# Kernel tuning notes

Measured on AMD Instinct MI355X. Metric: run time of the kernel, lower is better.

The kernel has to match this reference:

```python
import jax, jax.numpy as jnp
import numpy as np

B, S, V, H = 256, 1024, 256, 256


def setup_inputs() -> dict:
    key = jax.random.key(0)
    ks = jax.random.split(key, 12)
    s = 1.0 / np.sqrt(H)
    def u(k, shape):
        return jax.random.uniform(k, shape, jnp.float32, -s, s)
    return {
        "x": jax.random.normal(ks[0], (B, S, V), jnp.float32),
        "w_ih0": u(ks[1], (4 * H, V)),
        "w_hh0": u(ks[2], (4 * H, H)),
        "b_ih0": u(ks[3], (4 * H,)),
        "b_hh0": u(ks[4], (4 * H,)),
        "w_ih1": u(ks[5], (4 * H, H)),
        "w_hh1": u(ks[6], (4 * H, H)),
        "b_ih1": u(ks[7], (4 * H,)),
        "b_hh1": u(ks[8], (4 * H,)),
        "fc_w": u(ks[9], (V, H)),
        "fc_b": u(ks[10], (V,)),
    }


def _lstm_layer(inp, w_ih, w_hh, b_ih, b_hh):
    # inp: [B, S, D]. Precompute input contribution for all timesteps (big GEMM),
    # then scan the recurrence (PyTorch gate order: i, f, g, o).
    pre = jnp.einsum('bsd,gd->bsg', inp, w_ih) + b_ih + b_hh  # [B, S, 4H]
    h0 = jnp.zeros((inp.shape[0], w_hh.shape[1]), inp.dtype)
    c0 = jnp.zeros_like(h0)

    def step(carry, p):
        h, c = carry
        g = p + h @ w_hh.T  # [B, 4H]
        i, f, gg, o = jnp.split(g, 4, axis=-1)
        c = jax.nn.sigmoid(f) * c + jax.nn.sigmoid(i) * jnp.tanh(gg)
        h = jax.nn.sigmoid(o) * jnp.tanh(c)
        return (h, c), h

    _, hs = jax.lax.scan(step, (h0, c0), pre.transpose(1, 0, 2))  # hs: [S, B, H]
    return hs.transpose(1, 0, 2)


def reference(x, w_ih0, w_hh0, b_ih0, b_hh0, w_ih1, w_hh1, b_ih1, b_hh1, fc_w, fc_b):
    h1 = _lstm_layer(x, w_ih0, w_hh0, b_ih0, b_hh0)
    h2 = _lstm_layer(h1, w_ih1, w_hh1, b_ih1, b_hh1)
    logits = jnp.einsum('bsh,vh->bsv', h2, fc_w) + fc_b
    return jax.nn.log_softmax(logits, axis=-1)
```

## Files before the change

kernel.cpp:

```cpp
#include <hip/hip_runtime.h>
#include <cstdint>
#include <cstddef>


typedef __attribute__((ext_vector_type(8))) short bf16x8;
typedef __attribute__((ext_vector_type(4))) float f32x4;
typedef unsigned long long ull;

#define DEVFN __device__ __forceinline__

constexpr unsigned SENT = 0xFFFFFFFFu;

DEVFN unsigned short f2bf(float f) {
  union { float f; unsigned u; } v; v.f = f;
  unsigned r = v.u + 0x7FFFu + ((v.u >> 16) & 1u);
  return (unsigned short)(r >> 16);
}
DEVFN float sigm(float x) {
  return __builtin_amdgcn_rcpf(1.f + exp2f(x * -1.442695041f));
}
DEVFN float tanh2(float x) {
  return 1.f - 2.f * __builtin_amdgcn_rcpf(1.f + exp2f(x * 2.885390082f));
}
DEVFN ull aload64(const ull* p) {
  return __hip_atomic_load(p, __ATOMIC_RELAXED, __HIP_MEMORY_SCOPE_AGENT);
}
DEVFN void astore64(ull* p, ull v) {
  __hip_atomic_store(p, v, __ATOMIC_RELAXED, __HIP_MEMORY_SCOPE_AGENT);
}
DEVFN bf16x8 fragu(ull a, ull b) {
  union { ull u[2]; bf16x8 f; } t; t.u[0] = a; t.u[1] = b; return t.f;
}
DEVFN bf16x8 frag4(uint4 u) { union { uint4 u; bf16x8 f; } t; t.u = u; return t.f; }

#define KEEP8(a0,a1,a2,a3,a4,a5,a6,a7) \
  asm volatile("" : "+v"(a0), "+v"(a1), "+v"(a2), "+v"(a3), \
                    "+v"(a4), "+v"(a5), "+v"(a6), "+v"(a7))

__global__ void pack_w(const float* __restrict__ w, unsigned short* __restrict__ dst) {
  int bid = blockIdx.x;
  int lane = threadIdx.x;
  int col = (bid >> 3) * 16 + (lane & 15);
  int k0  = (bid & 7) * 32 + (lane >> 4) * 8;
  const float* src = w + (size_t)col * 256 + k0;
  unsigned short* d = dst + ((size_t)bid * 64 + lane) * 8;
#pragma unroll
  for (int j = 0; j < 8; ++j) d[j] = f2bf(src[j]);
}

__global__ void pack_x(const float* __restrict__ x, unsigned short* __restrict__ xp) {
  int bid = blockIdx.x, lane = threadIdx.x;
  int tc = bid & 7, kt = (bid >> 3) & 7, m = bid >> 6;
  int row = lane & 15, hi = lane >> 4;
  for (int t = tc * 128; t < tc * 128 + 128; ++t) {
    const float* s = x + ((size_t)(16 * m + row) * 1024 + t) * 256 + kt * 32 + hi * 8;
    float4 f0 = *(const float4*)s;
    float4 f1 = *(const float4*)(s + 4);
    uint4 o;
    o.x = f2bf(f0.x) | ((unsigned)f2bf(f0.y) << 16);
    o.y = f2bf(f0.z) | ((unsigned)f2bf(f0.w) << 16);
    o.z = f2bf(f1.x) | ((unsigned)f2bf(f1.y) << 16);
    o.w = f2bf(f1.z) | ((unsigned)f2bf(f1.w) << 16);
    *(uint4*)(xp + ((((size_t)t * 16 + m) * 8 + kt) * 64 + lane) * 8) = o;
  }
}

__global__ __attribute__((amdgpu_flat_work_group_size(64, 64),
                          amdgpu_waves_per_eu(1, 1)))
void lstm_dual(
    const unsigned short* __restrict__ xp,
    const unsigned short* __restrict__ Wih0, const unsigned short* __restrict__ Whh0,
    const float* __restrict__ bih0, const float* __restrict__ bhh0,
    const unsigned short* __restrict__ Wih1, const unsigned short* __restrict__ Whh1,
    const float* __restrict__ bih1, const float* __restrict__ bhh1,
    unsigned short* __restrict__ h1f, unsigned short* __restrict__ h2f)
{
  __shared__ unsigned short tl[16][24];
  const int lane = threadIdx.x;
  const int bid  = (int)blockIdx.x;
  const int m = bid & 15;
  const int L = (bid >> 4) & 1;
  const int w = bid >> 5;
  const int u = w * 16 + (lane & 15);
  const bool ownlane = (((lane >> 4) >> 1) == (w & 1));
  const int  mykt = w >> 1;

  const unsigned short* Wih = L ? Wih1 : Wih0;
  const unsigned short* Whh = L ? Whh1 : Whh0;
  const float* bihp = L ? bih1 : bih0;
  const float* bhhp = L ? bhh1 : bhh0;

  bf16x8 bwih[4][8], bwhh[4][8];
#pragma unroll
  for (int g = 0; g < 4; ++g)
#pragma unroll
    for (int kt = 0; kt < 8; ++kt) {
      bwih[g][kt] = *(const bf16x8*)(Wih + ((((size_t)(g * 16 + w)) * 8 + kt) * 64 + lane) * 8);
      bwhh[g][kt] = *(const bf16x8*)(Whh + ((((size_t)(g * 16 + w)) * 8 + kt) * 64 + lane) * 8);
    }
#pragma unroll
  for (int g = 0; g < 4; ++g) {
    KEEP8(bwih[g][0], bwih[g][1], bwih[g][2], bwih[g][3],
          bwih[g][4], bwih[g][5], bwih[g][6], bwih[g][7]);
    KEEP8(bwhh[g][0], bwhh[g][1], bwhh[g][2], bwhh[g][3],
          bwhh[g][4], bwhh[g][5], bwhh[g][6], bwhh[g][7]);
  }

  float bias[4];
#pragma unroll
  for (int g = 0; g < 4; ++g) bias[g] = bihp[g * 256 + u] + bhhp[g * 256 + u];

  float c[4] = {0.f, 0.f, 0.f, 0.f};

  constexpr int TSTEP_U = 16384;
  constexpr int TSTEP_X = 8192;

  if (!L) {
    const ull* hrd  = (const ull*)h1f + m * 1024 + lane * 2;
    const ull* hrd2 = hrd + 512;
    ull* hwr = (ull*)h1f + m * 1024 + mykt * 128 + lane * 2;
    const uint4* xq  = (const uint4*)xp + m * 512 + lane;
    const uint4* xq2 = xq + 256;

    uint4 xpre[8];
#pragma unroll
    for (int kt = 0; kt < 4; ++kt) { xpre[kt] = xq[kt * 64]; xpre[4 + kt] = xq2[kt * 64]; }
    xq += TSTEP_X; xq2 += TSTEP_X;

    for (int t = 0; t < 1024; ++t) {
      ull hv[16];
      if (t > 0) {
#pragma unroll
        for (int kt = 0; kt < 4; ++kt) {
          hv[2*kt]     = aload64(hrd  + kt * 128);
          hv[2*kt + 1] = aload64(hrd  + kt * 128 + 1);
          hv[8 + 2*kt]     = aload64(hrd2 + kt * 128);
          hv[8 + 2*kt + 1] = aload64(hrd2 + kt * 128 + 1);
        }
      }

      f32x4 acc[4];
#pragma unroll
      for (int g = 0; g < 4; ++g) acc[g] = (f32x4){0.f, 0.f, 0.f, 0.f};
#pragma unroll
      for (int kt = 0; kt < 8; ++kt) {
        bf16x8 a = frag4(xpre[kt]);
#pragma unroll
        for (int g = 0; g < 4; ++g)
          acc[g] = __builtin_amdgcn_mfma_f32_16x16x32_bf16(a, bwih[g][kt], acc[g], 0, 0, 0);
      }

      if (t > 0) {
        int rounds = 0;
        while (true) {
          bool bad = false;
#pragma unroll
          for (int i = 0; i < 16; ++i) bad = bad || ((unsigned)hv[i] == SENT);
          if (!__any(bad)) break;
          if (++rounds > 8) __builtin_amdgcn_s_sleep(1);
#pragma unroll
          for (int kt = 0; kt < 4; ++kt) {
            hv[2*kt]     = aload64(hrd  + kt * 128);
            hv[2*kt + 1] = aload64(hrd  + kt * 128 + 1);
            hv[8 + 2*kt]     = aload64(hrd2 + kt * 128);
            hv[8 + 2*kt + 1] = aload64(hrd2 + kt * 128 + 1);
          }
        }
#pragma unroll
        for (int kt = 0; kt < 8; ++kt) {
          bf16x8 a = fragu(hv[kt < 4 ? 2*kt : 2*kt], hv[kt < 4 ? 2*kt+1 : 2*kt+1]);
#pragma unroll
          for (int g = 0; g < 4; ++g)
            acc[g] = __builtin_amdgcn_mfma_f32_16x16x32_bf16(a, bwhh[g][kt], acc[g], 0, 0, 0);
        }
        hrd += TSTEP_U; hrd2 += TSTEP_U;
      }

      float hq[4];
#pragma unroll
      for (int q = 0; q < 4; ++q) {
        float ia = acc[0][q] + bias[0];
        float fa = acc[1][q] + bias[1];
        float ga = acc[2][q] + bias[2];
        float oa = acc[3][q] + bias[3];
        c[q] = sigm(fa) * c[q] + sigm(ia) * tanh2(ga);
        hq[q] = sigm(oa) * tanh2(c[q]);
      }
#pragma unroll
      for (int q = 0; q < 4; ++q)
        tl[(lane >> 4) * 4 + q][lane & 15] = f2bf(hq[q]);
      uint4 nown = *(const uint4*)(&tl[lane & 15][((lane >> 4) & 1) * 8]);
      if (ownlane) {
        astore64(hwr,     ((ull)nown.y << 32) | nown.x);
        astore64(hwr + 1, ((ull)nown.w << 32) | nown.z);
      }
      hwr += TSTEP_U;

      if (t < 1023) {
#pragma unroll
        for (int kt = 0; kt < 4; ++kt) { xpre[kt] = xq[kt * 64]; xpre[4 + kt] = xq2[kt * 64]; }
        xq += TSTEP_X; xq2 += TSTEP_X;
      }
    }
  } else {
    const ull* prd  = (const ull*)h1f + m * 1024 + lane * 2;
    const ull* prd2 = prd + 512;
    const ull* hrd  = (const ull*)h2f + m * 1024 + lane * 2;
    const ull* hrd2 = hrd + 512;
    ull* hwr = (ull*)h2f + m * 1024 + mykt * 128 + lane * 2;

    for (int t = 0; t < 1024; ++t) {
      ull p1[16], hv[16];
#pragma unroll
      for (int kt = 0; kt < 4; ++kt) {
        p1[2*kt]     = aload64(prd  + kt * 128);
        p1[2*kt + 1] = aload64(prd  + kt * 128 + 1);
        p1[8 + 2*kt]     = aload64(prd2 + kt * 128);
        p1[8 + 2*kt + 1] = aload64(prd2 + kt * 128 + 1);
      }
      if (t > 0) {
#pragma unroll
        for (int kt = 0; kt < 4; ++kt) {
          hv[2*kt]     = aload64(hrd  + kt * 128);
          hv[2*kt + 1] = aload64(hrd  + kt * 128 + 1);
          hv[8 + 2*kt]     = aload64(hrd2 + kt * 128);
          hv[8 + 2*kt + 1] = aload64(hrd2 + kt * 128 + 1);
        }
      }

      {
        int rounds = 0;
        while (true) {
          bool bad = false;
#pragma unroll
          for (int i = 0; i < 16; ++i) bad = bad || ((unsigned)p1[i] == SENT);
          if (!__any(bad)) break;
          if (++rounds > 8) __builtin_amdgcn_s_sleep(1);
#pragma unroll
          for (int kt = 0; kt < 4; ++kt) {
            p1[2*kt]     = aload64(prd  + kt * 128);
            p1[2*kt + 1] = aload64(prd  + kt * 128 + 1);
            p1[8 + 2*kt]     = aload64(prd2 + kt * 128);
            p1[8 + 2*kt + 1] = aload64(prd2 + kt * 128 + 1);
          }
        }
      }
      prd += TSTEP_U; prd2 += TSTEP_U;

      f32x4 acc[4];
#pragma unroll
      for (int g = 0; g < 4; ++g) acc[g] = (f32x4){0.f, 0.f, 0.f, 0.f};
#pragma unroll
      for (int kt = 0; kt < 8; ++kt) {
        bf16x8 a = fragu(p1[2*kt], p1[2*kt + 1]);
#pragma unroll
        for (int g = 0; g < 4; ++g)
          acc[g] = __builtin_amdgcn_mfma_f32_16x16x32_bf16(a, bwih[g][kt], acc[g], 0, 0, 0);
      }

      if (t > 0) {
        int rounds = 0;
        while (true) {
          bool bad = false;
#pragma unroll
          for (int i = 0; i < 16; ++i) bad = bad || ((unsigned)hv[i] == SENT);
          if (!__any(bad)) break;
          if (++rounds > 8) __builtin_amdgcn_s_sleep(1);
#pragma unroll
          for (int kt = 0; kt < 4; ++kt) {
            hv[2*kt]     = aload64(hrd  + kt * 128);
            hv[2*kt + 1] = aload64(hrd  + kt * 128 + 1);
            hv[8 + 2*kt]     = aload64(hrd2 + kt * 128);
            hv[8 + 2*kt + 1] = aload64(hrd2 + kt * 128 + 1);
          }
        }
#pragma unroll
        for (int kt = 0; kt < 8; ++kt) {
          bf16x8 a = fragu(hv[2*kt], hv[2*kt + 1]);
#pragma unroll
          for (int g = 0; g < 4; ++g)
            acc[g] = __builtin_amdgcn_mfma_f32_16x16x32_bf16(a, bwhh[g][kt], acc[g], 0, 0, 0);
        }
        hrd += TSTEP_U; hrd2 += TSTEP_U;
      }

      float hq[4];
#pragma unroll
      for (int q = 0; q < 4; ++q) {
        float ia = acc[0][q] + bias[0];
        float fa = acc[1][q] + bias[1];
        float ga = acc[2][q] + bias[2];
        float oa = acc[3][q] + bias[3];
        c[q] = sigm(fa) * c[q] + sigm(ia) * tanh2(ga);
        hq[q] = sigm(oa) * tanh2(c[q]);
      }
#pragma unroll
      for (int q = 0; q < 4; ++q)
        tl[(lane >> 4) * 4 + q][lane & 15] = f2bf(hq[q]);
      uint4 nown = *(const uint4*)(&tl[lane & 15][((lane >> 4) & 1) * 8]);
      if (ownlane) {
        astore64(hwr,     ((ull)nown.y << 32) | nown.x);
        astore64(hwr + 1, ((ull)nown.w << 32) | nown.z);
      }
      hwr += TSTEP_U;
    }
  }
}

__global__ __launch_bounds__(256, 1) void fc_lsm(
    const unsigned short* __restrict__ h2f,
    const unsigned short* __restrict__ Bp,
    const float* __restrict__ fcb,
    float* __restrict__ out)
{
  const int tid = threadIdx.x;
  const int wid = tid >> 6, lane = tid & 63;
  const int t = blockIdx.x >> 2;
  const int mloc = (blockIdx.x & 3) * 4 + wid;

  f32x4 acc[16];
#pragma unroll
  for (int nt = 0; nt < 16; ++nt) acc[nt] = (f32x4){0.f, 0.f, 0.f, 0.f};

#pragma unroll
  for (int kt = 0; kt < 8; ++kt) {
    bf16x8 a = *(const bf16x8*)(h2f + ((((size_t)t * 16 + mloc) * 8 + kt) * 64 + lane) * 8);
#pragma unroll
    for (int nt = 0; nt < 16; ++nt) {
      bf16x8 b = *(const bf16x8*)(Bp + (((size_t)nt * 8 + kt) * 64 + lane) * 8);
      acc[nt] = __builtin_amdgcn_mfma_f32_16x16x32_bf16(a, b, acc[nt], 0, 0, 0);
    }
  }
#pragma unroll
  for (int nt = 0; nt < 16; ++nt) {
    float bias = fcb[nt * 16 + (lane & 15)];
#pragma unroll
    for (int q = 0; q < 4; ++q) acc[nt][q] += bias;
  }

  float mx[4] = {-1e30f, -1e30f, -1e30f, -1e30f};
#pragma unroll
  for (int nt = 0; nt < 16; ++nt)
#pragma unroll
    for (int q = 0; q < 4; ++q) mx[q] = fmaxf(mx[q], acc[nt][q]);
#pragma unroll
  for (int d = 1; d < 16; d <<= 1)
#pragma unroll
    for (int q = 0; q < 4; ++q) mx[q] = fmaxf(mx[q], __shfl_xor(mx[q], d, 64));

  float sm[4] = {0.f, 0.f, 0.f, 0.f};
#pragma unroll
  for (int nt = 0; nt < 16; ++nt)
#pragma unroll
    for (int q = 0; q < 4; ++q) sm[q] += __expf(acc[nt][q] - mx[q]);
#pragma unroll
  for (int d = 1; d < 16; d <<= 1)
#pragma unroll
    for (int q = 0; q < 4; ++q) sm[q] += __shfl_xor(sm[q], d, 64);

  float lse[4];
#pragma unroll
  for (int q = 0; q < 4; ++q) lse[q] = mx[q] + __logf(sm[q]);

#pragma unroll
  for (int nt = 0; nt < 16; ++nt) {
#pragma unroll
    for (int q = 0; q < 4; ++q) {
      int b = mloc * 16 + (lane >> 4) * 4 + q;
      out[((size_t)b * 1024 + t) * 256 + nt * 16 + (lane & 15)] = acc[nt][q] - lse[q];
    }
  }
}

__global__ void fill_marker(float* out, size_t nvals) {
  size_t i = (size_t)blockIdx.x * blockDim.x + threadIdx.x;
  if (i < nvals) out[i] = -7777.0f;
}

extern "C" void kernel_launch(void* const* d_in, const int* in_sizes, int n_in,
                              void* d_out, int out_size, void* d_ws, size_t ws_size,
                              hipStream_t stream)
{
  (void)in_sizes; (void)n_in;
  const float* x    = (const float*)d_in[0];
  const float* wih0 = (const float*)d_in[1];
  const float* whh0 = (const float*)d_in[2];
  const float* bih0 = (const float*)d_in[3];
  const float* bhh0 = (const float*)d_in[4];
  const float* wih1 = (const float*)d_in[5];
  const float* whh1 = (const float*)d_in[6];
  const float* bih1 = (const float*)d_in[7];
  const float* bhh1 = (const float*)d_in[8];
  const float* fcw  = (const float*)d_in[9];
  const float* fcb  = (const float*)d_in[10];
  float* out = (float*)d_out;

  const size_t o_wp0i = 0;
  const size_t o_wp0h = o_wp0i + 524288;
  const size_t o_wp1i = o_wp0h + 524288;
  const size_t o_wp1h = o_wp1i + 524288;
  const size_t o_fcp  = o_wp1h + 524288;
  const size_t o_xp   = o_fcp  + 131072;
  const size_t o_h1f  = o_xp   + 134217728;
  const size_t o_h2f  = o_h1f  + 134217728;
  const size_t need   = o_h2f  + 134217728;

  if (ws_size < need) {
    size_t nv = (size_t)out_size;
    fill_marker<<<(unsigned)((nv + 1023) / 1024), 1024, 0, stream>>>(out, nv);
    return;
  }

  char* ws = (char*)d_ws;
  unsigned short* wp0i = (unsigned short*)(ws + o_wp0i);
  unsigned short* wp0h = (unsigned short*)(ws + o_wp0h);
  unsigned short* wp1i = (unsigned short*)(ws + o_wp1i);
  unsigned short* wp1h = (unsigned short*)(ws + o_wp1h);
  unsigned short* fcp  = (unsigned short*)(ws + o_fcp);
  unsigned short* xp   = (unsigned short*)(ws + o_xp);
  unsigned short* h1f  = (unsigned short*)(ws + o_h1f);
  unsigned short* h2f  = (unsigned short*)(ws + o_h2f);

  pack_w<<<512, 64, 0, stream>>>(wih0, wp0i);
  pack_w<<<512, 64, 0, stream>>>(whh0, wp0h);
  pack_w<<<512, 64, 0, stream>>>(wih1, wp1i);
  pack_w<<<512, 64, 0, stream>>>(whh1, wp1h);
  pack_w<<<128, 64, 0, stream>>>(fcw,  fcp);
  pack_x<<<1024, 64, 0, stream>>>(x, xp);

  hipMemsetAsync(h1f, 0xFF, 134217728, stream);
  hipMemsetAsync(h2f, 0xFF, 134217728, stream);

  lstm_dual<<<512, 64, 0, stream>>>(xp, wp0i, wp0h, bih0, bhh0,
                                    wp1i, wp1h, bih1, bhh1, h1f, h2f);

  fc_lsm<<<4096, 256, 0, stream>>>(h2f, fcp, fcb, out);
}
```

Baseline: 3.789 ms.

## Replace full-length hidden-state buffers with 16-slot rings and progress-based flow control

```diff
diff --git a/kernel.cpp b/kernel.cpp
--- a/kernel.cpp
+++ b/kernel.cpp
@@ -9,7 +9,8 @@
 
 #define DEVFN __device__ __forceinline__
 
-constexpr unsigned SENT = 0xFFFFFFFFu;
+constexpr unsigned SENT  = 0xFFFFFFFFu;
+constexpr ull      SENTU = 0xFFFFFFFFFFFFFFFFull;
 
 DEVFN unsigned short f2bf(float f) {
   union { float f; unsigned u; } v; v.f = f;
@@ -22,6 +23,12 @@
 DEVFN float tanh2(float x) {
   return 1.f - 2.f * __builtin_amdgcn_rcpf(1.f + exp2f(x * 2.885390082f));
 }
+DEVFN unsigned aload(const unsigned* p) {
+  return __hip_atomic_load(p, __ATOMIC_RELAXED, __HIP_MEMORY_SCOPE_AGENT);
+}
+DEVFN void astore(unsigned* p, unsigned v) {
+  __hip_atomic_store(p, v, __ATOMIC_RELAXED, __HIP_MEMORY_SCOPE_AGENT);
+}
 DEVFN ull aload64(const ull* p) {
   return __hip_atomic_load(p, __ATOMIC_RELAXED, __HIP_MEMORY_SCOPE_AGENT);
 }
@@ -32,10 +39,6 @@
   union { ull u[2]; bf16x8 f; } t; t.u[0] = a; t.u[1] = b; return t.f;
 }
 DEVFN bf16x8 frag4(uint4 u) { union { uint4 u; bf16x8 f; } t; t.u = u; return t.f; }
-
-#define KEEP8(a0,a1,a2,a3,a4,a5,a6,a7) \
-  asm volatile("" : "+v"(a0), "+v"(a1), "+v"(a2), "+v"(a3), \
-                    "+v"(a4), "+v"(a5), "+v"(a6), "+v"(a7))
 
 __global__ void pack_w(const float* __restrict__ w, unsigned short* __restrict__ dst) {
   int bid = blockIdx.x;
@@ -73,8 +76,10 @@
     const float* __restrict__ bih0, const float* __restrict__ bhh0,
     const unsigned short* __restrict__ Wih1, const unsigned short* __restrict__ Whh1,
     const float* __restrict__ bih1, const float* __restrict__ bhh1,
-    unsigned short* __restrict__ h1f, unsigned short* __restrict__ h2f)
+    ull* __restrict__ h1r, ull* __restrict__ h2r,
+    unsigned short* __restrict__ h2lin, unsigned* __restrict__ prog)
 {
+  __shared__ uint4 ldsW[2048];
   __shared__ unsigned short tl[16][24];
   const int lane = threadIdx.x;
   const int bid  = (int)blockIdx.x;
@@ -89,22 +94,21 @@
   const unsigned short* Whh = L ? Whh1 : Whh0;
   const float* bihp = L ? bih1 : bih0;
   const float* bhhp = L ? bhh1 : bhh0;
-
-  bf16x8 bwih[4][8], bwhh[4][8];
+  ull* ringo = L ? h2r : h1r;
+
 #pragma unroll
   for (int g = 0; g < 4; ++g)
 #pragma unroll
-    for (int kt = 0; kt < 8; ++kt) {
-      bwih[g][kt] = *(const bf16x8*)(Wih + ((((size_t)(g * 16 + w)) * 8 + kt) * 64 + lane) * 8);
+    for (int kt = 0; kt < 8; ++kt)
+      ldsW[(g * 8 + kt) * 64 + lane] =
+          *(const uint4*)(Wih + ((((size_t)(g * 16 + w)) * 8 + kt) * 64 + lane) * 8);
+
+  bf16x8 bwhh[4][8];
+#pragma unroll
+  for (int g = 0; g < 4; ++g)
+#pragma unroll
+    for (int kt = 0; kt < 8; ++kt)
       bwhh[g][kt] = *(const bf16x8*)(Whh + ((((size_t)(g * 16 + w)) * 8 + kt) * 64 + lane) * 8);
-    }
-#pragma unroll
-  for (int g = 0; g < 4; ++g) {
-    KEEP8(bwih[g][0], bwih[g][1], bwih[g][2], bwih[g][3],
-          bwih[g][4], bwih[g][5], bwih[g][6], bwih[g][7]);
-    KEEP8(bwhh[g][0], bwhh[g][1], bwhh[g][2], bwhh[g][3],
-          bwhh[g][4], bwhh[g][5], bwhh[g][6], bwhh[g][7]);
-  }
 
   float bias[4];
 #pragma unroll
@@ -112,42 +116,67 @@
 
   float c[4] = {0.f, 0.f, 0.f, 0.f};
 
-  constexpr int TSTEP_U = 16384;
-  constexpr int TSTEP_X = 8192;
+  const int mbase = m * 1024 + lane * 2;
+  const int obase = m * 1024 + mykt * 128 + lane * 2;
+  const uint4* ldsWp = ldsW;
 
   if (!L) {
-    const ull* hrd  = (const ull*)h1f + m * 1024 + lane * 2;
-    const ull* hrd2 = hrd + 512;
-    ull* hwr = (ull*)h1f + m * 1024 + mykt * 128 + lane * 2;
-    const uint4* xq  = (const uint4*)xp + m * 512 + lane;
-    const uint4* xq2 = xq + 256;
-
-    uint4 xpre[8];
-#pragma unroll
-    for (int kt = 0; kt < 4; ++kt) { xpre[kt] = xq[kt * 64]; xpre[4 + kt] = xq2[kt * 64]; }
-    xq += TSTEP_X; xq2 += TSTEP_X;
+    const unsigned* progm = prog + m * 16;
+    const uint4* xq = (const uint4*)xp + m * 512 + lane;
+    uint4 xcur[8], xnext[8];
+#pragma unroll
+    for (int kt = 0; kt < 4; ++kt) { xcur[kt] = xq[kt * 64]; xcur[4 + kt] = xq[256 + kt * 64]; }
+    xq += 8192;
 
     for (int t = 0; t < 1024; ++t) {
+      const int slot  = (t & 15) << 14;
+      const int slotp = ((t - 1) & 15) << 14;
+      const int slot2 = ((t + 2) & 15) << 14;
+
+      unsigned progv = 0;
+      if (t >= 14 && t < 1022) progv = aload(progm);
+
+      if (t < 1023) {
+#pragma unroll
+        for (int kt = 0; kt < 4; ++kt) { xnext[kt] = xq[kt * 64]; xnext[4 + kt] = xq[256 + kt * 64]; }
+        xq += 8192;
+      }
+
       ull hv[16];
+      const ull* hb  = ringo + slotp + mbase;
+      const ull* hb2 = hb + 512;
       if (t > 0) {
 #pragma unroll
         for (int kt = 0; kt < 4; ++kt) {
-          hv[2*kt]     = aload64(hrd  + kt * 128);
-          hv[2*kt + 1] = aload64(hrd  + kt * 128 + 1);
-          hv[8 + 2*kt]     = aload64(hrd2 + kt * 128);
-          hv[8 + 2*kt + 1] = aload64(hrd2 + kt * 128 + 1);
-        }
-      }
-
+          hv[2*kt]     = aload64(hb  + kt * 128);
+          hv[2*kt + 1] = aload64(hb  + kt * 128 + 1);
+          hv[8 + 2*kt]     = aload64(hb2 + kt * 128);
+          hv[8 + 2*kt + 1] = aload64(hb2 + kt * 128 + 1);
+        }
+      }
+
+      asm volatile("" : "+v"(ldsWp));
       f32x4 acc[4];
 #pragma unroll
       for (int g = 0; g < 4; ++g) acc[g] = (f32x4){0.f, 0.f, 0.f, 0.f};
 #pragma unroll
       for (int kt = 0; kt < 8; ++kt) {
-        bf16x8 a = frag4(xpre[kt]);
-#pragma unroll
-        for (int g = 0; g < 4; ++g)
-          acc[g] = __builtin_amdgcn_mfma_f32_16x16x32_bf16(a, bwih[g][kt], acc[g], 0, 0, 0);
+        bf16x8 a = frag4(xcur[kt]);
+#pragma unroll
+        for (int g = 0; g < 4; ++g) {
+          bf16x8 b = frag4(ldsWp[(g * 8 + kt) * 64 + lane]);
+          acc[g] = __builtin_amdgcn_mfma_f32_16x16x32_bf16(a, b, acc[g], 0, 0, 0);
+        }
+      }
+
+      if (t < 1022) {
+        if (t >= 14) {
+          while ((int)progv < t - 13) { __builtin_amdgcn_s_sleep(1); progv = aload(progm); }
+        }
+        if (ownlane) {
+          ull* sa = ringo + slot2 + obase;
+          astore64(sa, SENTU); astore64(sa + 1, SENTU);
+        }
       }
 
       if (t > 0) {
@@ -160,20 +189,19 @@
           if (++rounds > 8) __builtin_amdgcn_s_sleep(1);
 #pragma unroll
           for (int kt = 0; kt < 4; ++kt) {
-            hv[2*kt]     = aload64(hrd  + kt * 128);
-            hv[2*kt + 1] = aload64(hrd  + kt * 128 + 1);
-            hv[8 + 2*kt]     = aload64(hrd2 + kt * 128);
-            hv[8 + 2*kt + 1] = aload64(hrd2 + kt * 128 + 1);
+            hv[2*kt]     = aload64(hb  + kt * 128);
+            hv[2*kt + 1] = aload64(hb  + kt * 128 + 1);
+            hv[8 + 2*kt]     = aload64(hb2 + kt * 128);
+            hv[8 + 2*kt + 1] = aload64(hb2 + kt * 128 + 1);
           }
         }
 #pragma unroll
         for (int kt = 0; kt < 8; ++kt) {
-          bf16x8 a = fragu(hv[kt < 4 ? 2*kt : 2*kt], hv[kt < 4 ? 2*kt+1 : 2*kt+1]);
+          bf16x8 a = fragu(hv[2*kt], hv[2*kt + 1]);
 #pragma unroll
           for (int g = 0; g < 4; ++g)
             acc[g] = __builtin_amdgcn_mfma_f32_16x16x32_bf16(a, bwhh[g][kt], acc[g], 0, 0, 0);
         }
-        hrd += TSTEP_U; hrd2 += TSTEP_U;
       }
 
       float hq[4];
@@ -191,40 +219,46 @@
         tl[(lane >> 4) * 4 + q][lane & 15] = f2bf(hq[q]);
       uint4 nown = *(const uint4*)(&tl[lane & 15][((lane >> 4) & 1) * 8]);
       if (ownlane) {
-        astore64(hwr,     ((ull)nown.y << 32) | nown.x);
-        astore64(hwr + 1, ((ull)nown.w << 32) | nown.z);
-      }
-      hwr += TSTEP_U;
-
-      if (t < 1023) {
-#pragma unroll
-        for (int kt = 0; kt < 4; ++kt) { xpre[kt] = xq[kt * 64]; xpre[4 + kt] = xq2[kt * 64]; }
-        xq += TSTEP_X; xq2 += TSTEP_X;
-      }
+        ull* dw = ringo + slot + obase;
+        astore64(dw,     ((ull)nown.y << 32) | nown.x);
+        astore64(dw + 1, ((ull)nown.w << 32) | nown.z);
+      }
+#pragma unroll
+      for (int kt = 0; kt < 8; ++kt) xcur[kt] = xnext[kt];
     }
   } else {
-    const ull* prd  = (const ull*)h1f + m * 1024 + lane * 2;
-    const ull* prd2 = prd + 512;
-    const ull* hrd  = (const ull*)h2f + m * 1024 + lane * 2;
-    const ull* hrd2 = hrd + 512;
-    ull* hwr = (ull*)h2f + m * 1024 + mykt * 128 + lane * 2;
+    unsigned* progm = prog + m * 16;
+    unsigned short* hl = h2lin + ((size_t)(m * 8 + mykt)) * 512 + lane * 8;
 
     for (int t = 0; t < 1024; ++t) {
+      const int slot  = (t & 15) << 14;
+      const int slotp = ((t - 1) & 15) << 14;
+      const int slot2 = ((t + 2) & 15) << 14;
+
+      if (t < 1022 && ownlane) {
+        ull* sa = ringo + slot2 + obase;
+        astore64(sa, SENTU); astore64(sa + 1, SENTU);
+      }
+
       ull p1[16], hv[16];
+      const ull* pb  = h1r + slot + mbase;
+      const ull* pb2 = pb + 512;
 #pragma unroll
       for (int kt = 0; kt < 4; ++kt) {
-        p1[2*kt]     = aload64(prd  + kt * 128);
-        p1[2*kt + 1] = aload64(prd  + kt * 128 + 1);
-        p1[8 + 2*kt]     = aload64(prd2 + kt * 128);
-        p1[8 + 2*kt + 1] = aload64(prd2 + kt * 128 + 1);
-      }
+        p1[2*kt]     = aload64(pb  + kt * 128);
+        p1[2*kt + 1] = aload64(pb  + kt * 128 + 1);
+        p1[8 + 2*kt]     = aload64(pb2 + kt * 128);
+        p1[8 + 2*kt + 1] = aload64(pb2 + kt * 128 + 1);
+      }
+      const ull* hb  = ringo + slotp + mbase;
+      const ull* hb2 = hb + 512;
       if (t > 0) {
 #pragma unroll
         for (int kt = 0; kt < 4; ++kt) {
-          hv[2*kt]     = aload64(hrd  + kt * 128);
-          hv[2*kt + 1] = aload64(hrd  + kt * 128 + 1);
-          hv[8 + 2*kt]     = aload64(hrd2 + kt * 128);
-          hv[8 + 2*kt + 1] = aload64(hrd2 + kt * 128 + 1);
+          hv[2*kt]     = aload64(hb  + kt * 128);
+          hv[2*kt + 1] = aload64(hb  + kt * 128 + 1);
+          hv[8 + 2*kt]     = aload64(hb2 + kt * 128);
+          hv[8 + 2*kt + 1] = aload64(hb2 + kt * 128 + 1);
         }
       }
 
@@ -238,15 +272,15 @@
           if (++rounds > 8) __builtin_amdgcn_s_sleep(1);
 #pragma unroll
           for (int kt = 0; kt < 4; ++kt) {
-            p1[2*kt]     = aload64(prd  + kt * 128);
-            p1[2*kt + 1] = aload64(prd  + kt * 128 + 1);
-            p1[8 + 2*kt]     = aload64(prd2 + kt * 128);
-            p1[8 + 2*kt + 1] = aload64(prd2 + kt * 128 + 1);
+            p1[2*kt]     = aload64(pb  + kt * 128);
+            p1[2*kt + 1] = aload64(pb  + kt * 128 + 1);
+            p1[8 + 2*kt]     = aload64(pb2 + kt * 128);
+            p1[8 + 2*kt + 1] = aload64(pb2 + kt * 128 + 1);
           }
         }
       }
-      prd += TSTEP_U; prd2 += TSTEP_U;
-
+
+      asm volatile("" : "+v"(ldsWp));
       f32x4 acc[4];
 #pragma unroll
       for (int g = 0; g < 4; ++g) acc[g] = (f32x4){0.f, 0.f, 0.f, 0.f};
@@ -254,8 +288,10 @@
       for (int kt = 0; kt < 8; ++kt) {
         bf16x8 a = fragu(p1[2*kt], p1[2*kt + 1]);
 #pragma unroll
-        for (int g = 0; g < 4; ++g)
-          acc[g] = __builtin_amdgcn_mfma_f32_16x16x32_bf16(a, bwih[g][kt], acc[g], 0, 0, 0);
+        for (int g = 0; g < 4; ++g) {
+          bf16x8 b = frag4(ldsWp[(g * 8 + kt) * 64 + lane]);
+          acc[g] = __builtin_amdgcn_mfma_f32_16x16x32_bf16(a, b, acc[g], 0, 0, 0);
+        }
       }
 
       if (t > 0) {
@@ -268,12 +304,16 @@
           if (++rounds > 8) __builtin_amdgcn_s_sleep(1);
 #pragma unroll
           for (int kt = 0; kt < 4; ++kt) {
-            hv[2*kt]     = aload64(hrd  + kt * 128);
-            hv[2*kt + 1] = aload64(hrd  + kt * 128 + 1);
-            hv[8 + 2*kt]     = aload64(hrd2 + kt * 128);
-            hv[8 + 2*kt + 1] = aload64(hrd2 + kt * 128 + 1);
+            hv[2*kt]     = aload64(hb  + kt * 128);
+            hv[2*kt + 1] = aload64(hb  + kt * 128 + 1);
+            hv[8 + 2*kt]     = aload64(hb2 + kt * 128);
+            hv[8 + 2*kt + 1] = aload64(hb2 + kt * 128 + 1);
           }
         }
+      }
+      if (w == 0 && lane == 0) astore(progm, (unsigned)t);
+
+      if (t > 0) {
 #pragma unroll
         for (int kt = 0; kt < 8; ++kt) {
           bf16x8 a = fragu(hv[2*kt], hv[2*kt + 1]);
@@ -281,7 +321,6 @@
           for (int g = 0; g < 4; ++g)
             acc[g] = __builtin_amdgcn_mfma_f32_16x16x32_bf16(a, bwhh[g][kt], acc[g], 0, 0, 0);
         }
-        hrd += TSTEP_U; hrd2 += TSTEP_U;
       }
 
       float hq[4];
@@ -299,10 +338,12 @@
         tl[(lane >> 4) * 4 + q][lane & 15] = f2bf(hq[q]);
       uint4 nown = *(const uint4*)(&tl[lane & 15][((lane >> 4) & 1) * 8]);
       if (ownlane) {
-        astore64(hwr,     ((ull)nown.y << 32) | nown.x);
-        astore64(hwr + 1, ((ull)nown.w << 32) | nown.z);
-      }
-      hwr += TSTEP_U;
+        ull* dw = ringo + slot + obase;
+        astore64(dw,     ((ull)nown.y << 32) | nown.x);
+        astore64(dw + 1, ((ull)nown.w << 32) | nown.z);
+        *(uint4*)hl = nown;
+      }
+      hl += 65536;
     }
   }
 }
@@ -400,10 +441,12 @@
   const size_t o_wp1i = o_wp0h + 524288;
   const size_t o_wp1h = o_wp1i + 524288;
   const size_t o_fcp  = o_wp1h + 524288;
-  const size_t o_xp   = o_fcp  + 131072;
-  const size_t o_h1f  = o_xp   + 134217728;
-  const size_t o_h2f  = o_h1f  + 134217728;
-  const size_t need   = o_h2f  + 134217728;
+  const size_t o_prog = o_fcp  + 131072;
+  const size_t o_h1r  = o_prog + 65536;
+  const size_t o_h2r  = o_h1r  + 2097152;
+  const size_t o_xp   = o_h2r  + 2097152;
+  const size_t o_h2l  = o_xp   + 134217728;
+  const size_t need   = o_h2l  + 134217728;
 
   if (ws_size < need) {
     size_t nv = (size_t)out_size;
@@ -417,9 +460,11 @@
   unsigned short* wp1i = (unsigned short*)(ws + o_wp1i);
   unsigned short* wp1h = (unsigned short*)(ws + o_wp1h);
   unsigned short* fcp  = (unsigned short*)(ws + o_fcp);
+  unsigned*       prog = (unsigned*)(ws + o_prog);
+  ull*            h1r  = (ull*)(ws + o_h1r);
+  ull*            h2r  = (ull*)(ws + o_h2r);
   unsigned short* xp   = (unsigned short*)(ws + o_xp);
-  unsigned short* h1f  = (unsigned short*)(ws + o_h1f);
-  unsigned short* h2f  = (unsigned short*)(ws + o_h2f);
+  unsigned short* h2l  = (unsigned short*)(ws + o_h2l);
 
   pack_w<<<512, 64, 0, stream>>>(wih0, wp0i);
   pack_w<<<512, 64, 0, stream>>>(whh0, wp0h);
@@ -428,11 +473,12 @@
   pack_w<<<128, 64, 0, stream>>>(fcw,  fcp);
   pack_x<<<1024, 64, 0, stream>>>(x, xp);
 
-  hipMemsetAsync(h1f, 0xFF, 134217728, stream);
-  hipMemsetAsync(h2f, 0xFF, 134217728, stream);
+  hipMemsetAsync(prog, 0, 65536, stream);
+  hipMemsetAsync(h1r, 0xFF, 2097152, stream);
+  hipMemsetAsync(h2r, 0xFF, 2097152, stream);
 
   lstm_dual<<<512, 64, 0, stream>>>(xp, wp0i, wp0h, bih0, bhh0,
-                                    wp1i, wp1h, bih1, bhh1, h1f, h2f);
-
-  fc_lsm<<<4096, 256, 0, stream>>>(h2f, fcp, fcb, out);
-}
+                                    wp1i, wp1h, bih1, bhh1, h1r, h2r, h2l, prog);
+
+  fc_lsm<<<4096, 256, 0, stream>>>(h2l, fcp, fcb, out);
+}
```

New measurement: 4.007 ms. 5.7% more time.
